# Kernel optimization log

Hardware: AMD Instinct MI355X
Metric: run time of the kernel (lower is better)

## Reference

```python
import jax, jax.numpy as jnp
import numpy as np

NUM_LAYERS = 24
LN_EPS = 1e-5


def setup_inputs() -> dict:
    key = jax.random.key(0)
    ks = jax.random.split(key, 8)
    B, S = 256, 8192
    x = jax.random.uniform(ks[0], (B, S, 5), dtype=jnp.float32)
    # per-layer LayerNorm(4) params (torch default init: weight=1, bias=0; use
    # randomized values so the gather is non-trivial)
    ln_w = 1.0 + 0.1 * jax.random.normal(ks[1], (NUM_LAYERS, 4), dtype=jnp.float32)
    ln_b = 0.1 * jax.random.normal(ks[2], (NUM_LAYERS, 4), dtype=jnp.float32)
    # MLP 5 -> 64 -> 32 -> 1 (dropout inactive in eval mode)
    W1 = jax.random.normal(ks[3], (64, 5), dtype=jnp.float32) / np.sqrt(5)
    b1 = jnp.zeros((64,), dtype=jnp.float32)
    W2 = jax.random.normal(ks[4], (32, 64), dtype=jnp.float32) / np.sqrt(64)
    b2 = jnp.zeros((32,), dtype=jnp.float32)
    W3 = jax.random.normal(ks[5], (1, 32), dtype=jnp.float32) / np.sqrt(32)
    b3 = jnp.zeros((1,), dtype=jnp.float32)
    return {"x": x, "ln_w": ln_w, "ln_b": ln_b, "W1": W1, "b1": b1,
            "W2": W2, "b2": b2, "W3": W3, "b3": b3}


def reference(x, ln_w, ln_b, W1, b1, W2, b2, W3, b3):
    B, S, _ = x.shape
    x_flat = x.reshape(-1, 5)                      # [N, 5]
    layer_pos = x_flat[:, -1]                      # [N]
    layer_ids = jnp.clip((layer_pos * NUM_LAYERS).astype(jnp.int32), 0, NUM_LAYERS - 1)
    feats = x_flat[:, :4]                          # [N, 4]
    # vectorized per-token LayerNorm: gather per-token gamma/beta by layer id
    mean = jnp.mean(feats, axis=-1, keepdims=True)
    var = jnp.mean(jnp.square(feats - mean), axis=-1, keepdims=True)  # biased, as torch LN
    normed = (feats - mean) * jax.lax.rsqrt(var + LN_EPS)
    normed = normed * ln_w[layer_ids] + ln_b[layer_ids]               # [N, 4]
    x_norm = jnp.concatenate([normed, layer_pos[:, None]], axis=1)    # [N, 5]
    h = jax.nn.relu(x_norm @ W1.T + b1)            # [N, 64]
    h = jax.nn.relu(h @ W2.T + b2)                 # [N, 32]
    scores = h @ W3.T + b3                         # [N, 1]
    return scores.reshape(B, S)
```

## Files before the change

kernel.cpp:

```cpp
#include <hip/hip_runtime.h>
#include <hip/hip_bf16.h>
#include <stdint.h>

#define NUM_LAYERS 24
#define LN_EPS 1e-5f
#define N_ROWS (256 * 8192)
#define ROWS_PER_ITER 32
#define NUM_ITERS (N_ROWS / ROWS_PER_ITER)
#define NUM_BLOCKS 2048

typedef __attribute__((ext_vector_type(8)))  short bf16x8;
typedef __attribute__((ext_vector_type(16))) float f32x16;

__device__ __forceinline__ uint32_t pk_bf16(float lo, float hi) {
    __hip_bfloat162 h2 = __float22bfloat162_rn(float2{lo, hi});
    uint32_t u;
    __builtin_memcpy(&u, &h2, 4);
    return u;
}

union FragU { bf16x8 f; uint32_t u[4]; };

__device__ __forceinline__ bf16x8 make_frag(uint32_t d0, uint32_t d1,
                                            uint32_t d2, uint32_t d3) {
    FragU fu;
    fu.u[0] = d0; fu.u[1] = d1; fu.u[2] = d2; fu.u[3] = d3;
    return fu.f;
}

__device__ __forceinline__ int sigma_k(int p) {
    int hh = (p >> 2) & 1;
    int base = (p & 31) - 4 * hh;
    int r = (base & 3) + 4 * (base >> 3);
    return 32 * (p >> 5) + 16 * (r >> 3) + 8 * hh + (r & 7);
}

__global__ __launch_bounds__(256, 4) void router_mfma(
    const float* __restrict__ x,
    const float* __restrict__ ln_w,
    const float* __restrict__ ln_b,
    const float* __restrict__ W1,
    const float* __restrict__ b1,
    const float* __restrict__ W2,
    const float* __restrict__ b2,
    const float* __restrict__ W3,
    const float* __restrict__ b3,
    float* __restrict__ out)
{
    __shared__ float s_ln[NUM_LAYERS * 8];
    const int t = threadIdx.x;
    if (t < NUM_LAYERS * 4) {
        int lid = t >> 2, c = t & 3;
        s_ln[lid * 8 + c]     = ln_w[t];
        s_ln[lid * 8 + 4 + c] = ln_b[t];
    }
    __syncthreads();

    const int lane = t & 63;
    const int wid  = t >> 6;
    const int n32  = lane & 31;
    const int h    = lane >> 5;

    bf16x8 a1f[2];
#pragma unroll
    for (int mt = 0; mt < 2; ++mt) {
        int p = mt * 32 + n32;
        int k = sigma_k(p);
        float w0 = W1[k * 5 + 0], w1 = W1[k * 5 + 1], w2 = W1[k * 5 + 2];
        float w3 = W1[k * 5 + 3], w4 = W1[k * 5 + 4];
        float bc = b1[k];
        uint32_t d0 = pk_bf16(w0, w1);
        uint32_t d1 = pk_bf16(w2, w3);
        uint32_t d2 = pk_bf16(w4, bc);
        if (h) { d0 = 0; d1 = 0; d2 = 0; }
        a1f[mt] = make_frag(d0, d1, d2, 0);
    }

    bf16x8 w2f[4];
#pragma unroll
    for (int kt = 0; kt < 4; ++kt) {
        const float* wp = W2 + n32 * 64 + kt * 16 + h * 8;
        const float4 lo = *(const float4*)(wp);
        const float4 hi = *(const float4*)(wp + 4);
        w2f[kt] = make_frag(pk_bf16(lo.x, lo.y), pk_bf16(lo.z, lo.w),
                            pk_bf16(hi.x, hi.y), pk_bf16(hi.z, hi.w));
    }

    float w3n[16], b2n[16];
#pragma unroll
    for (int r = 0; r < 16; ++r) {
        const int n = (r & 3) + 8 * (r >> 2) + 4 * h;
        w3n[r] = W3[n];
        b2n[r] = b2[n];
    }
    const float b3v = b3[0];

    const int total_waves = NUM_BLOCKS * 4;
    const int w = blockIdx.x * 4 + wid;

    int it = w;
    const float* xp0 = x + (size_t)(it * ROWS_PER_ITER + n32) * 5;
    float f0 = xp0[0], f1 = xp0[1], f2 = xp0[2], f3 = xp0[3], lp = xp0[4];

    while (true) {
        const int nit = it + total_waves;
        const bool more = nit < NUM_ITERS;
        const float* nxp = x + (size_t)((more ? nit : it) * ROWS_PER_ITER + n32) * 5;
        const float nf0 = nxp[0], nf1 = nxp[1], nf2 = nxp[2], nf3 = nxp[3],
                    nlp = nxp[4];

        const int rowBase = it * ROWS_PER_ITER;

        int lid = (int)(lp * (float)NUM_LAYERS);
        lid = lid < 0 ? 0 : (lid > NUM_LAYERS - 1 ? NUM_LAYERS - 1 : lid);

        const float m  = (f0 + f1 + f2 + f3) * 0.25f;
        const float d0 = f0 - m, d1 = f1 - m, d2 = f2 - m, d3 = f3 - m;
        const float var = (d0 * d0 + d1 * d1 + d2 * d2 + d3 * d3) * 0.25f;
        const float r   = rsqrtf(var + LN_EPS);

        const float4 g  = *(const float4*)(s_ln + lid * 8);
        const float4 bb = *(const float4*)(s_ln + lid * 8 + 4);

        const float xn0 = fmaf(d0 * r, g.x, bb.x);
        const float xn1 = fmaf(d1 * r, g.y, bb.y);
        const float xn2 = fmaf(d2 * r, g.z, bb.z);
        const float xn3 = fmaf(d3 * r, g.w, bb.w);

        uint32_t e0 = pk_bf16(xn0, xn1);
        uint32_t e1 = pk_bf16(xn2, xn3);
        uint32_t e2 = pk_bf16(lp, 1.0f);
        if (h) { e0 = 0; e1 = 0; e2 = 0; }
        const bf16x8 b1f = make_frag(e0, e1, e2, 0);

        f32x16 z;
#pragma unroll
        for (int i = 0; i < 16; ++i) z[i] = 0.0f;
        f32x16 c1a = __builtin_amdgcn_mfma_f32_32x32x16_bf16(a1f[0], b1f, z, 0, 0, 0);
        f32x16 c1b = __builtin_amdgcn_mfma_f32_32x32x16_bf16(a1f[1], b1f, z, 0, 0, 0);

        bf16x8 h1f[4];
#pragma unroll
        for (int kt = 0; kt < 4; ++kt) {
            const f32x16& c1 = (kt < 2) ? c1a : c1b;
            const int roff = 8 * (kt & 1);
            uint32_t dw[4];
#pragma unroll
            for (int d = 0; d < 4; ++d) {
                float va = fmaxf(c1[roff + 2 * d], 0.0f);
                float vb = fmaxf(c1[roff + 2 * d + 1], 0.0f);
                dw[d] = pk_bf16(va, vb);
            }
            h1f[kt] = make_frag(dw[0], dw[1], dw[2], dw[3]);
        }

        f32x16 c2;
#pragma unroll
        for (int i = 0; i < 16; ++i) c2[i] = b2n[i];
#pragma unroll
        for (int kt = 0; kt < 4; ++kt)
            c2 = __builtin_amdgcn_mfma_f32_32x32x16_bf16(w2f[kt], h1f[kt], c2, 0, 0, 0);

        float part = 0.0f;
#pragma unroll
        for (int rr = 0; rr < 16; ++rr)
            part = fmaf(fmaxf(c2[rr], 0.0f), w3n[rr], part);
        part += __shfl_xor(part, 32, 64);
        if (!h) out[rowBase + n32] = part + b3v;

        if (!more) break;
        it = nit;
        f0 = nf0; f1 = nf1; f2 = nf2; f3 = nf3; lp = nlp;
    }
}

extern "C" void kernel_launch(void* const* d_in, const int* in_sizes, int n_in,
                              void* d_out, int out_size, void* d_ws, size_t ws_size,
                              hipStream_t stream) {
    const float* x    = (const float*)d_in[0];
    const float* ln_w = (const float*)d_in[1];
    const float* ln_b = (const float*)d_in[2];
    const float* W1   = (const float*)d_in[3];
    const float* b1   = (const float*)d_in[4];
    const float* W2   = (const float*)d_in[5];
    const float* b2   = (const float*)d_in[6];
    const float* W3   = (const float*)d_in[7];
    const float* b3   = (const float*)d_in[8];
    float* out = (float*)d_out;

    router_mfma<<<NUM_BLOCKS, 256, 0, stream>>>(x, ln_w, ln_b, W1, b1, W2, b2,
                                                W3, b3, out);
}
```

Baseline: 122.6 us.

## Process 64 rows per wave with all lanes doing LayerNorm and packed FP32 epilogue

Each wave now handles 64 rows per iteration instead of 32. All 64 lanes load and normalize a row, and the upper half's bf16 fragments are shuffled down so two MFMA tiles run back to back. This removes the redundant LayerNorm work and loads on the upper half-wave, and lets every lane write an output. The ReLU, bias and W3 dot epilogue now uses two-wide float vectors so the compiler can emit packed FP32 math. The extra tile raises register pressure, so launch bounds drop to 3 blocks per CU.

```diff
diff --git a/kernel.cpp b/kernel.cpp
--- a/kernel.cpp
+++ b/kernel.cpp
@@ -5,12 +5,13 @@
 #define NUM_LAYERS 24
 #define LN_EPS 1e-5f
 #define N_ROWS (256 * 8192)
-#define ROWS_PER_ITER 32
+#define ROWS_PER_ITER 64
 #define NUM_ITERS (N_ROWS / ROWS_PER_ITER)
 #define NUM_BLOCKS 2048
 
 typedef __attribute__((ext_vector_type(8)))  short bf16x8;
 typedef __attribute__((ext_vector_type(16))) float f32x16;
+typedef __attribute__((ext_vector_type(2)))  float f32x2;
 
 __device__ __forceinline__ uint32_t pk_bf16(float lo, float hi) {
     __hip_bfloat162 h2 = __float22bfloat162_rn(float2{lo, hi});
@@ -35,7 +36,7 @@
     return 32 * (p >> 5) + 16 * (r >> 3) + 8 * hh + (r & 7);
 }
 
-__global__ __launch_bounds__(256, 4) void router_mfma(
+__global__ __launch_bounds__(256, 3) void router_mfma(
     const float* __restrict__ x,
     const float* __restrict__ ln_w,
     const float* __restrict__ ln_b,
@@ -86,26 +87,33 @@
                             pk_bf16(hi.x, hi.y), pk_bf16(hi.z, hi.w));
     }
 
-    float w3n[16], b2n[16];
-#pragma unroll
-    for (int r = 0; r < 16; ++r) {
+    f32x2 w3p[8], b2p[8];
+#pragma unroll
+    for (int r2 = 0; r2 < 8; ++r2) {
+        const int r = 2 * r2;
         const int n = (r & 3) + 8 * (r >> 2) + 4 * h;
-        w3n[r] = W3[n];
-        b2n[r] = b2[n];
+        w3p[r2] = f32x2{W3[n], W3[n + 1]};
+        b2p[r2] = f32x2{b2[n], b2[n + 1]};
     }
     const float b3v = b3[0];
+
+    f32x16 zf;
+#pragma unroll
+    for (int i = 0; i < 16; ++i) zf[i] = 0.0f;
+    const f32x2 z2 = {0.0f, 0.0f};
 
     const int total_waves = NUM_BLOCKS * 4;
     const int w = blockIdx.x * 4 + wid;
 
     int it = w;
-    const float* xp0 = x + (size_t)(it * ROWS_PER_ITER + n32) * 5;
+    const float* xp0 = x + (size_t)(it * ROWS_PER_ITER + lane) * 5;
     float f0 = xp0[0], f1 = xp0[1], f2 = xp0[2], f3 = xp0[3], lp = xp0[4];
 
     while (true) {
         const int nit = it + total_waves;
         const bool more = nit < NUM_ITERS;
-        const float* nxp = x + (size_t)((more ? nit : it) * ROWS_PER_ITER + n32) * 5;
+        const float* nxp =
+            x + (size_t)((more ? nit : it) * ROWS_PER_ITER + lane) * 5;
         const float nf0 = nxp[0], nf1 = nxp[1], nf2 = nxp[2], nf3 = nxp[3],
                     nlp = nxp[4];
 
@@ -127,46 +135,58 @@
         const float xn2 = fmaf(d2 * r, g.z, bb.z);
         const float xn3 = fmaf(d3 * r, g.w, bb.w);
 
-        uint32_t e0 = pk_bf16(xn0, xn1);
-        uint32_t e1 = pk_bf16(xn2, xn3);
-        uint32_t e2 = pk_bf16(lp, 1.0f);
-        if (h) { e0 = 0; e1 = 0; e2 = 0; }
-        const bf16x8 b1f = make_frag(e0, e1, e2, 0);
-
-        f32x16 z;
-#pragma unroll
-        for (int i = 0; i < 16; ++i) z[i] = 0.0f;
-        f32x16 c1a = __builtin_amdgcn_mfma_f32_32x32x16_bf16(a1f[0], b1f, z, 0, 0, 0);
-        f32x16 c1b = __builtin_amdgcn_mfma_f32_32x32x16_bf16(a1f[1], b1f, z, 0, 0, 0);
-
-        bf16x8 h1f[4];
-#pragma unroll
-        for (int kt = 0; kt < 4; ++kt) {
-            const f32x16& c1 = (kt < 2) ? c1a : c1b;
-            const int roff = 8 * (kt & 1);
-            uint32_t dw[4];
-#pragma unroll
-            for (int d = 0; d < 4; ++d) {
-                float va = fmaxf(c1[roff + 2 * d], 0.0f);
-                float vb = fmaxf(c1[roff + 2 * d + 1], 0.0f);
-                dw[d] = pk_bf16(va, vb);
+        const uint32_t e0 = pk_bf16(xn0, xn1);
+        const uint32_t e1 = pk_bf16(xn2, xn3);
+        const uint32_t e2 = pk_bf16(lp, 1.0f);
+        const uint32_t x0 = __shfl_xor((int)e0, 32, 64);
+        const uint32_t x1 = __shfl_xor((int)e1, 32, 64);
+        const uint32_t x2 = __shfl_xor((int)e2, 32, 64);
+
+        const bf16x8 bf_t0 = make_frag(h ? 0u : e0, h ? 0u : e1, h ? 0u : e2, 0u);
+        const bf16x8 bf_t1 = make_frag(h ? 0u : x0, h ? 0u : x1, h ? 0u : x2, 0u);
+
+        float res[2];
+#pragma unroll
+        for (int tile = 0; tile < 2; ++tile) {
+            const bf16x8 b1f = tile ? bf_t1 : bf_t0;
+
+            f32x16 c1a = __builtin_amdgcn_mfma_f32_32x32x16_bf16(a1f[0], b1f, zf, 0, 0, 0);
+            f32x16 c1b = __builtin_amdgcn_mfma_f32_32x32x16_bf16(a1f[1], b1f, zf, 0, 0, 0);
+
+            bf16x8 h1f[4];
+#pragma unroll
+            for (int kt = 0; kt < 4; ++kt) {
+                const f32x16& c1 = (kt < 2) ? c1a : c1b;
+                const int roff = 8 * (kt & 1);
+                uint32_t dw[4];
+#pragma unroll
+                for (int d = 0; d < 4; ++d) {
+                    f32x2 v = {c1[roff + 2 * d], c1[roff + 2 * d + 1]};
+                    v = __builtin_elementwise_max(v, z2);
+                    dw[d] = pk_bf16(v.x, v.y);
+                }
+                h1f[kt] = make_frag(dw[0], dw[1], dw[2], dw[3]);
             }
-            h1f[kt] = make_frag(dw[0], dw[1], dw[2], dw[3]);
+
+            f32x16 c2 = __builtin_amdgcn_mfma_f32_32x32x16_bf16(w2f[0], h1f[0], zf, 0, 0, 0);
+#pragma unroll
+            for (int kt = 1; kt < 4; ++kt)
+                c2 = __builtin_amdgcn_mfma_f32_32x32x16_bf16(w2f[kt], h1f[kt], c2, 0, 0, 0);
+
+            f32x2 acc = z2;
+#pragma unroll
+            for (int r2 = 0; r2 < 8; ++r2) {
+                f32x2 v = {c2[2 * r2], c2[2 * r2 + 1]};
+                v = v + b2p[r2];
+                v = __builtin_elementwise_max(v, z2);
+                acc = v * w3p[r2] + acc;
+            }
+            float part = acc.x + acc.y;
+            part += __shfl_xor(part, 32, 64);
+            res[tile] = part + b3v;
         }
 
-        f32x16 c2;
-#pragma unroll
-        for (int i = 0; i < 16; ++i) c2[i] = b2n[i];
-#pragma unroll
-        for (int kt = 0; kt < 4; ++kt)
-            c2 = __builtin_amdgcn_mfma_f32_32x32x16_bf16(w2f[kt], h1f[kt], c2, 0, 0, 0);
-
-        float part = 0.0f;
-#pragma unroll
-        for (int rr = 0; rr < 16; ++rr)
-            part = fmaf(fmaxf(c2[rr], 0.0f), w3n[rr], part);
-        part += __shfl_xor(part, 32, 64);
-        if (!h) out[rowBase + n32] = part + b3v;
+        out[rowBase + lane] = (h ? res[1] : res[0]) + 0.0f;
 
         if (!more) break;
         it = nit;
```

After: 117.7 us. 4.0% less time.
